# Optimization experiments

Hardware: AMD Instinct MI355X
Metric: run time of the kernel (lower is better)

The kernel has to match this reference:

```python
import jax, jax.numpy as jnp
import numpy as np

IN_FEATURES = 4096
OUT_FEATURES = 4096


def setup_inputs() -> dict:
    key = jax.random.key(0)
    k_x, k_w, k_b = jax.random.split(key, 3)
    inp = {
        "input": jax.random.normal(k_x, (4, 2048, IN_FEATURES), dtype=jnp.float32),
        # learned int8 weight table [out_features, in_features]
        "weight_int8": jax.random.randint(k_w, (OUT_FEATURES, IN_FEATURES), -128, 128, dtype=jnp.int32).astype(jnp.int8),
        # per-tensor dequant scales (scalars, as in the module buffers)
        "scale": jnp.asarray(0.01, dtype=jnp.float32),
        "x_scale": jnp.asarray(0.05, dtype=jnp.float32),
        "bias": jax.random.normal(k_b, (OUT_FEATURES,), dtype=jnp.float32) * 0.02,
    }
    return inp


def reference(input, weight_int8, scale, x_scale, bias):
    # --- quantize activations per-tensor to int8 (W8A8 path) ---
    x_int8 = jnp.clip(jnp.round(input / x_scale), -128, 127).astype(jnp.int8)
    in_shape = input.shape
    x_flat = x_int8.reshape(-1, in_shape[-1])  # [B*S, in]
    # contract x_flat[k] with weight_int8[n, k] -> [B*S, out]
    out_i32 = jax.lax.dot_general(
        x_flat, weight_int8,
        dimension_numbers=(((1,), (1,)), ((), ())),
        preferred_element_type=jnp.int32,
    )
    # --- dequant epilogue: combined scale, reshape, bias ---
    out = out_i32.astype(input.dtype) * (scale * x_scale)
    out = out.reshape(*in_shape[:-1], weight_int8.shape[0])
    out = out + bias
    return out
```

## Files before the change

### kernel.cpp

```cpp
#include <hip/hip_runtime.h>

#define KDIM 4096
#define NDIM 4096
#define BM 256
#define BN 256
#define BK 128
#define NTILE (KDIM / BK)
#define NPAIR (NTILE * 4)

using i32x4 = __attribute__((ext_vector_type(4))) int;

__device__ __forceinline__ void g2l16(const void* g, void* l) {
  __builtin_amdgcn_global_load_lds(
      (const __attribute__((address_space(1))) void*)g,
      (__attribute__((address_space(3))) void*)l,
      16, 0, 0);
}

__global__ void w8l_detect(const int* __restrict__ w32, int* __restrict__ flag) {
  __shared__ int s;
  const int t = threadIdx.x;
  if (t == 0) s = 1;
  __syncthreads();
  bool oob = false;
#pragma unroll
  for (int i = 0; i < 16; ++i) {
    int v = w32[t * 16 + i];
    if (v < -128 || v > 127) oob = true;
  }
  if (oob) atomicAnd(&s, 0);
  __syncthreads();
  if (t == 0) *flag = s;
}

__global__ void w8l_pack(const void* __restrict__ wsrc, const int* __restrict__ flag,
                         signed char* __restrict__ wq) {
  const int t = blockIdx.x * blockDim.x + threadIdx.x;
  if (*flag) {
    const int4* s = (const int4*)wsrc;
    int4 a = s[t * 4 + 0], b = s[t * 4 + 1], c = s[t * 4 + 2], d = s[t * 4 + 3];
    int4 o;
    o.x = (a.x & 255) | ((a.y & 255) << 8) | ((a.z & 255) << 16) | ((a.w & 255) << 24);
    o.y = (b.x & 255) | ((b.y & 255) << 8) | ((b.z & 255) << 16) | ((b.w & 255) << 24);
    o.z = (c.x & 255) | ((c.y & 255) << 8) | ((c.z & 255) << 16) | ((c.w & 255) << 24);
    o.w = (d.x & 255) | ((d.y & 255) << 8) | ((d.z & 255) << 16) | ((d.w & 255) << 24);
    ((int4*)wq)[t] = o;
  } else {
    ((int4*)wq)[t] = ((const int4*)wsrc)[t];
  }
}

__global__ void w8l_quant(const float* __restrict__ x, const float* __restrict__ xs,
                          signed char* __restrict__ xq) {
  const int t = blockIdx.x * blockDim.x + threadIdx.x;
  const float s = *xs;
  const float4* x4 = (const float4*)x;
  int4 o;
  int* op = (int*)&o;
#pragma unroll
  for (int q = 0; q < 4; ++q) {
    float4 f = x4[t * 4 + q];
    int v0 = __float2int_rn(f.x / s);
    int v1 = __float2int_rn(f.y / s);
    int v2 = __float2int_rn(f.z / s);
    int v3 = __float2int_rn(f.w / s);
    v0 = v0 < -128 ? -128 : (v0 > 127 ? 127 : v0);
    v1 = v1 < -128 ? -128 : (v1 > 127 ? 127 : v1);
    v2 = v2 < -128 ? -128 : (v2 > 127 ? 127 : v2);
    v3 = v3 < -128 ? -128 : (v3 > 127 ? 127 : v3);
    op[q] = (v0 & 255) | ((v1 & 255) << 8) | ((v2 & 255) << 16) | ((v3 & 255) << 24);
  }
  ((int4*)xq)[t] = o;
}

__global__ __launch_bounds__(512, 2) void w8l_gemm8(
    const signed char* __restrict__ Aq, const signed char* __restrict__ Wq,
    const float* __restrict__ scale, const float* __restrict__ xscale,
    const float* __restrict__ bias, float* __restrict__ out, int nbn) {
  __shared__ signed char lds[131072];

  const int tid = threadIdx.x;
  const int lane = tid & 63;
  const int wid = tid >> 6;
  const int wr = wid >> 2;
  const int wc = wid & 3;
  const int l15 = lane & 15;
  const int l4 = lane >> 4;

  const int nwg = gridDim.x;
  const int cpx = nwg >> 3;
  const int bid = blockIdx.x;
  const int swz = (bid & 7) * cpx + (bid >> 3);
  const int bm = swz / nbn, bn = swz % nbn;
  const int m0 = bm * BM, n0 = bn * BN;

  const unsigned lin = (unsigned)tid * 16u;
  const unsigned r_in = lin >> 7;
  const unsigned c16 = (lin >> 4) & 7;
  const unsigned swcol = ((c16 ^ (r_in & 7)) << 4);
  const signed char* agp = Aq + (size_t)(m0 + r_in) * KDIM + swcol;
  const signed char* wgp = Wq + (size_t)(n0 + r_in) * KDIM + swcol;
  const unsigned ldsoff_thr = r_in * 128u + c16 * 16u;

#define ISSUE_PAIR(q)                                                          \
  do {                                                                         \
    const int q_ = (q);                                                        \
    if (q_ < NPAIR) {                                                          \
      const int tile_ = q_ >> 2;                                               \
      const int mat_ = (q_ >> 1) & 1;                                          \
      const int rb_ = (q_ & 1) * 128;                                          \
      const signed char* gp_ = (mat_ ? wgp : agp) + ((size_t)rb_ << 12) + tile_ * 128; \
      signed char* lp_ = lds + (unsigned)(tile_ & 1) * 65536u +                \
                         (unsigned)mat_ * 32768u + (unsigned)rb_ * 128u + ldsoff_thr; \
      g2l16(gp_, lp_);                                                         \
      g2l16(gp_ + ((size_t)64 << 12), lp_ + 8192);                             \
    }                                                                          \
  } while (0)

#define LDFRAG(base, row, s) \
  (*(const i32x4*)((base) + (row) * 128 + ((((s)*4 + l4) ^ ((row) & 7)) * 16)))

  i32x4 acc[8][4] = {};

  ISSUE_PAIR(0); ISSUE_PAIR(1); ISSUE_PAIR(2); ISSUE_PAIR(3); ISSUE_PAIR(4);
  asm volatile("s_waitcnt vmcnt(2)" ::: "memory");
  __builtin_amdgcn_s_barrier();

#pragma unroll 1
  for (int kt = 0; kt < NTILE; ++kt) {
    const signed char* Ab = &lds[(kt & 1) * 65536];
    const signed char* Bb = Ab + 32768;
    i32x4 a0[4][2], a1[4][2], b01[2][2], b23[2][2];

#pragma unroll
    for (int i = 0; i < 4; ++i)
#pragma unroll
      for (int s = 0; s < 2; ++s) a0[i][s] = LDFRAG(Ab, wr * 128 + i * 16 + l15, s);
#pragma unroll
    for (int j = 0; j < 2; ++j)
#pragma unroll
      for (int s = 0; s < 2; ++s) b01[j][s] = LDFRAG(Bb, wc * 64 + j * 16 + l15, s);
    ISSUE_PAIR(4 * kt + 5);
    __builtin_amdgcn_s_barrier();
    asm volatile("s_waitcnt lgkmcnt(0)" ::: "memory");
    __builtin_amdgcn_sched_barrier(0);
    __builtin_amdgcn_s_setprio(1);
#pragma unroll
    for (int i = 0; i < 4; ++i)
#pragma unroll
      for (int j = 0; j < 2; ++j)
#pragma unroll
        for (int s = 0; s < 2; ++s)
          acc[i][j] = __builtin_amdgcn_mfma_i32_16x16x64_i8(a0[i][s], b01[j][s], acc[i][j], 0, 0, 0);
    __builtin_amdgcn_s_setprio(0);
    __builtin_amdgcn_s_barrier();

#pragma unroll
    for (int j = 0; j < 2; ++j)
#pragma unroll
      for (int s = 0; s < 2; ++s) b23[j][s] = LDFRAG(Bb, wc * 64 + (j + 2) * 16 + l15, s);
    ISSUE_PAIR(4 * kt + 6);
    __builtin_amdgcn_s_barrier();
    asm volatile("s_waitcnt lgkmcnt(0)" ::: "memory");
    __builtin_amdgcn_sched_barrier(0);
    __builtin_amdgcn_s_setprio(1);
#pragma unroll
    for (int i = 0; i < 4; ++i)
#pragma unroll
      for (int j = 0; j < 2; ++j)
#pragma unroll
        for (int s = 0; s < 2; ++s)
          acc[i][j + 2] = __builtin_amdgcn_mfma_i32_16x16x64_i8(a0[i][s], b23[j][s], acc[i][j + 2], 0, 0, 0);
    __builtin_amdgcn_s_setprio(0);
    __builtin_amdgcn_s_barrier();

#pragma unroll
    for (int i = 0; i < 4; ++i)
#pragma unroll
      for (int s = 0; s < 2; ++s) a1[i][s] = LDFRAG(Ab, wr * 128 + (i + 4) * 16 + l15, s);
    ISSUE_PAIR(4 * kt + 7);
    __builtin_amdgcn_s_barrier();
    asm volatile("s_waitcnt lgkmcnt(0)" ::: "memory");
    __builtin_amdgcn_sched_barrier(0);
    __builtin_amdgcn_s_setprio(1);
#pragma unroll
    for (int i = 0; i < 4; ++i)
#pragma unroll
      for (int j = 0; j < 2; ++j)
#pragma unroll
        for (int s = 0; s < 2; ++s)
          acc[i + 4][j + 2] = __builtin_amdgcn_mfma_i32_16x16x64_i8(a1[i][s], b23[j][s], acc[i + 4][j + 2], 0, 0, 0);
    __builtin_amdgcn_s_setprio(0);
    __builtin_amdgcn_s_barrier();

    ISSUE_PAIR(4 * kt + 8);
    if (kt < NTILE - 2) {
      asm volatile("s_waitcnt vmcnt(2)" ::: "memory");
    } else {
      asm volatile("s_waitcnt vmcnt(0)" ::: "memory");
    }
    __builtin_amdgcn_s_barrier();
    __builtin_amdgcn_sched_barrier(0);
    __builtin_amdgcn_s_setprio(1);
#pragma unroll
    for (int i = 0; i < 4; ++i)
#pragma unroll
      for (int j = 0; j < 2; ++j)
#pragma unroll
        for (int s = 0; s < 2; ++s)
          acc[i + 4][j] = __builtin_amdgcn_mfma_i32_16x16x64_i8(a1[i][s], b01[j][s], acc[i + 4][j], 0, 0, 0);
    __builtin_amdgcn_s_setprio(0);
    __builtin_amdgcn_s_barrier();
  }

  const float cs = scale[0] * xscale[0];
#pragma unroll
  for (int j = 0; j < 4; ++j) {
    const int n = n0 + wc * 64 + j * 16 + l15;
    const float bj = bias[n];
#pragma unroll
    for (int i = 0; i < 8; ++i) {
      const int m = m0 + wr * 128 + i * 16 + l4 * 4;
      float* o = out + (size_t)m * NDIM + n;
#pragma unroll
      for (int v = 0; v < 4; ++v)
        o[(size_t)v * NDIM] = (float)acc[i][j][v] * cs + bj;
    }
  }
#undef ISSUE_PAIR
#undef LDFRAG
}

extern "C" void kernel_launch(void* const* d_in, const int* in_sizes, int n_in,
                              void* d_out, int out_size, void* d_ws, size_t ws_size,
                              hipStream_t stream) {
  const float* x = (const float*)d_in[0];
  const void* w = d_in[1];
  const float* scale = (const float*)d_in[2];
  const float* xscale = (const float*)d_in[3];
  const float* bias = (const float*)d_in[4];
  float* out = (float*)d_out;

  const int M = in_sizes[0] / KDIM;

  int* flag = (int*)d_ws;
  signed char* wq = (signed char*)d_ws + 256;
  signed char* aq = wq + (size_t)NDIM * KDIM;

  const size_t need = 256 + (size_t)NDIM * KDIM + (size_t)M * KDIM;
  if (ws_size < need) return;

  w8l_detect<<<1, 256, 0, stream>>>((const int*)w, flag);
  w8l_pack<<<(NDIM * KDIM / 16) / 256, 256, 0, stream>>>(w, flag, wq);
  w8l_quant<<<(M * KDIM / 16) / 256, 256, 0, stream>>>(x, xscale, aq);

  const int nbn = NDIM / BN;
  w8l_gemm8<<<(M / BM) * nbn, 512, 0, stream>>>(aq, wq, scale, xscale, bias, out, nbn);
}
```

Measured before the change: 186.4 us.

## Restructure GEMM main loop to whole-tile prefetch and skip raw weight copy

The GEMM main loop changes from four barrier-separated phases, each issuing a quarter of the next tile's loads, to one phase per K tile. That phase issues the whole next tile, waits on vmcnt, does a single barrier, loads all fragments from LDS and runs the four MFMA groups with lgkmcnt-staged waits. This cuts the number of workgroup barriers per iteration from eight to two but adds register pressure and a shallower prefetch. The pack kernel now exits early when the weight input is already int8, and the GEMM reads the raw weight buffer directly in that case, removing a full weight copy.

```diff
diff --git a/kernel.cpp b/kernel.cpp
--- a/kernel.cpp
+++ b/kernel.cpp
@@ -6,7 +6,6 @@
 #define BN 256
 #define BK 128
 #define NTILE (KDIM / BK)
-#define NPAIR (NTILE * 4)
 
 using i32x4 = __attribute__((ext_vector_type(4))) int;
 
@@ -35,19 +34,16 @@
 
 __global__ void w8l_pack(const void* __restrict__ wsrc, const int* __restrict__ flag,
                          signed char* __restrict__ wq) {
+  if (*flag == 0) return;
   const int t = blockIdx.x * blockDim.x + threadIdx.x;
-  if (*flag) {
-    const int4* s = (const int4*)wsrc;
-    int4 a = s[t * 4 + 0], b = s[t * 4 + 1], c = s[t * 4 + 2], d = s[t * 4 + 3];
-    int4 o;
-    o.x = (a.x & 255) | ((a.y & 255) << 8) | ((a.z & 255) << 16) | ((a.w & 255) << 24);
-    o.y = (b.x & 255) | ((b.y & 255) << 8) | ((b.z & 255) << 16) | ((b.w & 255) << 24);
-    o.z = (c.x & 255) | ((c.y & 255) << 8) | ((c.z & 255) << 16) | ((c.w & 255) << 24);
-    o.w = (d.x & 255) | ((d.y & 255) << 8) | ((d.z & 255) << 16) | ((d.w & 255) << 24);
-    ((int4*)wq)[t] = o;
-  } else {
-    ((int4*)wq)[t] = ((const int4*)wsrc)[t];
-  }
+  const int4* s = (const int4*)wsrc;
+  int4 a = s[t * 4 + 0], b = s[t * 4 + 1], c = s[t * 4 + 2], d = s[t * 4 + 3];
+  int4 o;
+  o.x = (a.x & 255) | ((a.y & 255) << 8) | ((a.z & 255) << 16) | ((a.w & 255) << 24);
+  o.y = (b.x & 255) | ((b.y & 255) << 8) | ((b.z & 255) << 16) | ((b.w & 255) << 24);
+  o.z = (c.x & 255) | ((c.y & 255) << 8) | ((c.z & 255) << 16) | ((c.w & 255) << 24);
+  o.w = (d.x & 255) | ((d.y & 255) << 8) | ((d.z & 255) << 16) | ((d.w & 255) << 24);
+  ((int4*)wq)[t] = o;
 }
 
 __global__ void w8l_quant(const float* __restrict__ x, const float* __restrict__ xs,
@@ -74,10 +70,14 @@
 }
 
 __global__ __launch_bounds__(512, 2) void w8l_gemm8(
-    const signed char* __restrict__ Aq, const signed char* __restrict__ Wq,
+    const signed char* __restrict__ Aq,
+    const signed char* __restrict__ Wraw, const signed char* __restrict__ Wpk,
+    const int* __restrict__ flag,
     const float* __restrict__ scale, const float* __restrict__ xscale,
     const float* __restrict__ bias, float* __restrict__ out, int nbn) {
   __shared__ signed char lds[131072];
+
+  const signed char* __restrict__ Wq = (*flag) ? Wpk : Wraw;
 
   const int tid = threadIdx.x;
   const int lane = tid & 63;
@@ -102,106 +102,93 @@
   const signed char* wgp = Wq + (size_t)(n0 + r_in) * KDIM + swcol;
   const unsigned ldsoff_thr = r_in * 128u + c16 * 16u;
 
-#define ISSUE_PAIR(q)                                                          \
-  do {                                                                         \
-    const int q_ = (q);                                                        \
-    if (q_ < NPAIR) {                                                          \
-      const int tile_ = q_ >> 2;                                               \
-      const int mat_ = (q_ >> 1) & 1;                                          \
-      const int rb_ = (q_ & 1) * 128;                                          \
-      const signed char* gp_ = (mat_ ? wgp : agp) + ((size_t)rb_ << 12) + tile_ * 128; \
-      signed char* lp_ = lds + (unsigned)(tile_ & 1) * 65536u +                \
-                         (unsigned)mat_ * 32768u + (unsigned)rb_ * 128u + ldsoff_thr; \
-      g2l16(gp_, lp_);                                                         \
-      g2l16(gp_ + ((size_t)64 << 12), lp_ + 8192);                             \
-    }                                                                          \
+#define ISSUE_TILE(t)                                                     \
+  do {                                                                    \
+    const int t_ = (t);                                                   \
+    const size_t koff_ = (size_t)t_ * BK;                                 \
+    signed char* lb_ = lds + (unsigned)(t_ & 1) * 65536u + ldsoff_thr;    \
+    _Pragma("unroll") for (int u = 0; u < 4; ++u)                         \
+      g2l16(agp + (size_t)(u * 64) * KDIM + koff_, lb_ + u * 8192);       \
+    _Pragma("unroll") for (int u = 0; u < 4; ++u)                         \
+      g2l16(wgp + (size_t)(u * 64) * KDIM + koff_, lb_ + 32768 + u * 8192); \
   } while (0)
 
-#define LDFRAG(base, row, s) \
-  (*(const i32x4*)((base) + (row) * 128 + ((((s)*4 + l4) ^ ((row) & 7)) * 16)))
+#define LDFRAG(base, row, sl) \
+  (*(const i32x4*)((base) + (row) * 128 + (((((sl) * 4) + l4) ^ ((row) & 7)) * 16)))
 
   i32x4 acc[8][4] = {};
 
-  ISSUE_PAIR(0); ISSUE_PAIR(1); ISSUE_PAIR(2); ISSUE_PAIR(3); ISSUE_PAIR(4);
-  asm volatile("s_waitcnt vmcnt(2)" ::: "memory");
-  __builtin_amdgcn_s_barrier();
+  ISSUE_TILE(0);
 
 #pragma unroll 1
   for (int kt = 0; kt < NTILE; ++kt) {
-    const signed char* Ab = &lds[(kt & 1) * 65536];
-    const signed char* Bb = Ab + 32768;
-    i32x4 a0[4][2], a1[4][2], b01[2][2], b23[2][2];
-
-#pragma unroll
-    for (int i = 0; i < 4; ++i)
-#pragma unroll
-      for (int s = 0; s < 2; ++s) a0[i][s] = LDFRAG(Ab, wr * 128 + i * 16 + l15, s);
-#pragma unroll
-    for (int j = 0; j < 2; ++j)
-#pragma unroll
-      for (int s = 0; s < 2; ++s) b01[j][s] = LDFRAG(Bb, wc * 64 + j * 16 + l15, s);
-    ISSUE_PAIR(4 * kt + 5);
-    __builtin_amdgcn_s_barrier();
-    asm volatile("s_waitcnt lgkmcnt(0)" ::: "memory");
-    __builtin_amdgcn_sched_barrier(0);
-    __builtin_amdgcn_s_setprio(1);
-#pragma unroll
-    for (int i = 0; i < 4; ++i)
-#pragma unroll
-      for (int j = 0; j < 2; ++j)
-#pragma unroll
-        for (int s = 0; s < 2; ++s)
-          acc[i][j] = __builtin_amdgcn_mfma_i32_16x16x64_i8(a0[i][s], b01[j][s], acc[i][j], 0, 0, 0);
-    __builtin_amdgcn_s_setprio(0);
-    __builtin_amdgcn_s_barrier();
-
-#pragma unroll
-    for (int j = 0; j < 2; ++j)
-#pragma unroll
-      for (int s = 0; s < 2; ++s) b23[j][s] = LDFRAG(Bb, wc * 64 + (j + 2) * 16 + l15, s);
-    ISSUE_PAIR(4 * kt + 6);
-    __builtin_amdgcn_s_barrier();
-    asm volatile("s_waitcnt lgkmcnt(0)" ::: "memory");
-    __builtin_amdgcn_sched_barrier(0);
-    __builtin_amdgcn_s_setprio(1);
-#pragma unroll
-    for (int i = 0; i < 4; ++i)
-#pragma unroll
-      for (int j = 0; j < 2; ++j)
-#pragma unroll
-        for (int s = 0; s < 2; ++s)
-          acc[i][j + 2] = __builtin_amdgcn_mfma_i32_16x16x64_i8(a0[i][s], b23[j][s], acc[i][j + 2], 0, 0, 0);
-    __builtin_amdgcn_s_setprio(0);
-    __builtin_amdgcn_s_barrier();
-
-#pragma unroll
-    for (int i = 0; i < 4; ++i)
-#pragma unroll
-      for (int s = 0; s < 2; ++s) a1[i][s] = LDFRAG(Ab, wr * 128 + (i + 4) * 16 + l15, s);
-    ISSUE_PAIR(4 * kt + 7);
-    __builtin_amdgcn_s_barrier();
-    asm volatile("s_waitcnt lgkmcnt(0)" ::: "memory");
-    __builtin_amdgcn_sched_barrier(0);
-    __builtin_amdgcn_s_setprio(1);
-#pragma unroll
-    for (int i = 0; i < 4; ++i)
-#pragma unroll
-      for (int j = 0; j < 2; ++j)
-#pragma unroll
-        for (int s = 0; s < 2; ++s)
-          acc[i + 4][j + 2] = __builtin_amdgcn_mfma_i32_16x16x64_i8(a1[i][s], b23[j][s], acc[i + 4][j + 2], 0, 0, 0);
-    __builtin_amdgcn_s_setprio(0);
-    __builtin_amdgcn_s_barrier();
-
-    ISSUE_PAIR(4 * kt + 8);
-    if (kt < NTILE - 2) {
-      asm volatile("s_waitcnt vmcnt(2)" ::: "memory");
+    if (kt + 1 < NTILE) {
+      ISSUE_TILE(kt + 1);
+      asm volatile("s_waitcnt vmcnt(8)" ::: "memory");
     } else {
       asm volatile("s_waitcnt vmcnt(0)" ::: "memory");
     }
     __builtin_amdgcn_s_barrier();
     __builtin_amdgcn_sched_barrier(0);
+
+    const signed char* Ab = &lds[(kt & 1) * 65536];
+    const signed char* Bb = Ab + 32768;
+    i32x4 a0[4][2], a1[4][2], b01[2][2], b23[2][2];
+
+#pragma unroll
+    for (int i = 0; i < 4; ++i)
+#pragma unroll
+      for (int s = 0; s < 2; ++s) a0[i][s] = LDFRAG(Ab, wr * 128 + i * 16 + l15, s);
+#pragma unroll
+    for (int j = 0; j < 2; ++j)
+#pragma unroll
+      for (int s = 0; s < 2; ++s) b01[j][s] = LDFRAG(Bb, wc * 64 + j * 16 + l15, s);
+    asm volatile("s_waitcnt lgkmcnt(0)" ::: "memory");
+    __builtin_amdgcn_sched_barrier(0);
+
+#pragma unroll
+    for (int j = 0; j < 2; ++j)
+#pragma unroll
+      for (int s = 0; s < 2; ++s) b23[j][s] = LDFRAG(Bb, wc * 64 + (j + 2) * 16 + l15, s);
+    __builtin_amdgcn_sched_barrier(0);
+#pragma unroll
+    for (int i = 0; i < 4; ++i)
+#pragma unroll
+      for (int s = 0; s < 2; ++s) a1[i][s] = LDFRAG(Ab, wr * 128 + (i + 4) * 16 + l15, s);
+    __builtin_amdgcn_sched_barrier(0);
+
     __builtin_amdgcn_s_setprio(1);
+#pragma unroll
+    for (int i = 0; i < 4; ++i)
+#pragma unroll
+      for (int j = 0; j < 2; ++j)
+#pragma unroll
+        for (int s = 0; s < 2; ++s)
+          acc[i][j] = __builtin_amdgcn_mfma_i32_16x16x64_i8(a0[i][s], b01[j][s], acc[i][j], 0, 0, 0);
+    __builtin_amdgcn_s_setprio(0);
+
+    asm volatile("s_waitcnt lgkmcnt(8)" ::: "memory");
+    __builtin_amdgcn_sched_barrier(0);
+    __builtin_amdgcn_s_setprio(1);
+#pragma unroll
+    for (int i = 0; i < 4; ++i)
+#pragma unroll
+      for (int j = 0; j < 2; ++j)
+#pragma unroll
+        for (int s = 0; s < 2; ++s)
+          acc[i][j + 2] = __builtin_amdgcn_mfma_i32_16x16x64_i8(a0[i][s], b23[j][s], acc[i][j + 2], 0, 0, 0);
+    __builtin_amdgcn_s_setprio(0);
+
+    asm volatile("s_waitcnt lgkmcnt(0)" ::: "memory");
+    __builtin_amdgcn_sched_barrier(0);
+    __builtin_amdgcn_s_setprio(1);
+#pragma unroll
+    for (int i = 0; i < 4; ++i)
+#pragma unroll
+      for (int j = 0; j < 2; ++j)
+#pragma unroll
+        for (int s = 0; s < 2; ++s)
+          acc[i + 4][j + 2] = __builtin_amdgcn_mfma_i32_16x16x64_i8(a1[i][s], b23[j][s], acc[i + 4][j + 2], 0, 0, 0);
 #pragma unroll
     for (int i = 0; i < 4; ++i)
 #pragma unroll
@@ -210,6 +197,7 @@
         for (int s = 0; s < 2; ++s)
           acc[i + 4][j] = __builtin_amdgcn_mfma_i32_16x16x64_i8(a1[i][s], b01[j][s], acc[i + 4][j], 0, 0, 0);
     __builtin_amdgcn_s_setprio(0);
+    __builtin_amdgcn_sched_barrier(0);
     __builtin_amdgcn_s_barrier();
   }
 
@@ -227,7 +215,7 @@
         o[(size_t)v * NDIM] = (float)acc[i][j][v] * cs + bj;
     }
   }
-#undef ISSUE_PAIR
+#undef ISSUE_TILE
 #undef LDFRAG
 }
 
@@ -255,5 +243,6 @@
   w8l_quant<<<(M * KDIM / 16) / 256, 256, 0, stream>>>(x, xscale, aq);
 
   const int nbn = NDIM / BN;
-  w8l_gemm8<<<(M / BM) * nbn, 512, 0, stream>>>(aq, wq, scale, xscale, bias, out, nbn);
-}
+  w8l_gemm8<<<(M / BM) * nbn, 512, 0, stream>>>(
+      aq, (const signed char*)w, wq, flag, scale, xscale, bias, out, nbn);
+}
```

Result: no change. 189.4 us (+1.6%).
